# Kernel optimization log

Measured on AMD Instinct MI355X. Metric: run time of the kernel, lower is better.

Reference implementation:

```python
import jax, jax.numpy as jnp
import numpy as np

EPS = 1e-8

def unit_projection(x):
    # project each embedding vector so its Fourier coefficients have unit magnitude
    f = jnp.fft.fft(x, axis=-1)
    f = f / jnp.maximum(jnp.abs(f), EPS)
    return jnp.real(jnp.fft.ifft(f, axis=-1))

def bind(a, b):
    return jnp.fft.irfft(jnp.fft.rfft(a, axis=-1) * jnp.fft.rfft(b, axis=-1), n=a.shape[-1], axis=-1)

def unbind(s, k):
    # k is unit-magnitude in Fourier domain, so its inverse is its conjugate
    return jnp.fft.irfft(jnp.fft.rfft(s, axis=-1) * jnp.conj(jnp.fft.rfft(k, axis=-1)), n=s.shape[-1], axis=-1)

def layer_norm(x, g, b):
    mu = jnp.mean(x, axis=-1, keepdims=True)
    var = jnp.var(x, axis=-1, keepdims=True)
    return (x - mu) * jax.lax.rsqrt(var + 1e-5) * g + b

def setup_inputs():
    key = jax.random.key(0)
    ks = jax.random.split(key, 12)
    B, S, D = 4, 2048, 1024
    sc = 1.0 / np.sqrt(D)
    inp = {
        'x': jax.random.normal(ks[0], (B, S, D), jnp.float32),
        'Wq': jax.random.normal(ks[1], (D, D), jnp.float32) * sc,
        'bq': jnp.zeros((D,), jnp.float32),
        'Wk': jax.random.normal(ks[2], (D, D), jnp.float32) * sc,
        'bk': jnp.zeros((D,), jnp.float32),
        'Wv': jax.random.normal(ks[3], (D, D), jnp.float32) * sc,
        'bv': jnp.zeros((D,), jnp.float32),
        'ln1_g': jnp.ones((D,), jnp.float32), 'ln1_b': jnp.zeros((D,), jnp.float32),
        'ln2_g': jnp.ones((D,), jnp.float32), 'ln2_b': jnp.zeros((D,), jnp.float32),
        'W1': jax.random.normal(ks[4], (D, 4 * D), jnp.float32) * sc,
        'b1': jnp.zeros((4 * D,), jnp.float32),
        'W2': jax.random.normal(ks[5], (4 * D, D), jnp.float32) * (1.0 / np.sqrt(4 * D)),
        'b2': jnp.zeros((D,), jnp.float32),
    }
    return inp

def reference(x, Wq, bq, Wk, bk, Wv, bv, ln1_g, ln1_b, ln2_g, ln2_b, W1, b1, W2, b2):
    h = layer_norm(x, ln1_g, ln1_b)
    q = unit_projection(h @ Wq + bq)
    k = unit_projection(h @ Wk + bk)
    v = unit_projection(h @ Wv + bv)
    s = jnp.cumsum(bind(k, v), axis=1)  # causal prefix-sum over sequence
    mixed = unbind(s, q)
    x = x + mixed  # dropout=0.0
    h2 = layer_norm(x, ln2_g, ln2_b)
    mlp = jax.nn.gelu(h2 @ W1 + b1, approximate=False) @ W2 + b2
    return x + mlp
```

## Files before the change

kernel.cpp:

```cpp
#include <hip/hip_runtime.h>
#include <cstdint>
#include <cstddef>

#define DD 1024
#define SSEQ 2048
#define NB 4
#define MROWS 8192
#define FBINS 513
#define FPAD 520
#define WFP 1152
#define NQKV 3456
#define NHID 4096
#define NCHUNK 128
#define SCHUNK 16

typedef _Float16 f16_t;
typedef _Float16 f16x8 __attribute__((ext_vector_type(8)));
typedef _Float16 f16x2 __attribute__((ext_vector_type(2)));
typedef float f32x4 __attribute__((ext_vector_type(4)));

__device__ __forceinline__ float2 cmul(float2 a, float2 b) {
  return make_float2(a.x * b.x - a.y * b.y, a.x * b.y + a.y * b.x);
}

__device__ __forceinline__ void async_cp16(const void* g, void* l) {
  __builtin_amdgcn_global_load_lds(
      (const __attribute__((address_space(1))) void*)g,
      (__attribute__((address_space(3))) void*)l, 16, 0, 0);
}

template <int N> __device__ __forceinline__ void vwait();
template <> __device__ __forceinline__ void vwait<0>() { asm volatile("s_waitcnt vmcnt(0)" ::: "memory"); }
template <> __device__ __forceinline__ void vwait<1>() { asm volatile("s_waitcnt vmcnt(1)" ::: "memory"); }
template <> __device__ __forceinline__ void vwait<2>() { asm volatile("s_waitcnt vmcnt(2)" ::: "memory"); }
template <> __device__ __forceinline__ void vwait<3>() { asm volatile("s_waitcnt vmcnt(3)" ::: "memory"); }
template <> __device__ __forceinline__ void vwait<4>() { asm volatile("s_waitcnt vmcnt(4)" ::: "memory"); }
template <> __device__ __forceinline__ void vwait<5>() { asm volatile("s_waitcnt vmcnt(5)" ::: "memory"); }
template <> __device__ __forceinline__ void vwait<6>() { asm volatile("s_waitcnt vmcnt(6)" ::: "memory"); }

__device__ __forceinline__ float fast_gelu(float val) {
  float av = __builtin_fabsf(val);
  float z = av * 0.70710678118654752f;
  float t = __builtin_amdgcn_rcpf(__builtin_fmaf(0.3275911f, z, 1.0f));
  float poly = t * __builtin_fmaf(t,
      __builtin_fmaf(t, __builtin_fmaf(t,
          __builtin_fmaf(t, 1.061405429f, -1.453152027f),
          1.421413741f), -0.284496736f), 0.254829592f);
  float e = __builtin_amdgcn_exp2f(z * z * -1.4426950408889634f);
  float w = poly * e;
  float r = fmaxf(val, 0.0f);
  return __builtin_fmaf(-0.5f * av, w, r);
}

__device__ __forceinline__ void fft1024(float2* bufA, float2* bufB,
                                        const float2* tw, int lt) {
  float2* s = bufA;
  float2* d = bufB;
  for (int m = 1; m < 1024; m <<= 1) {
#pragma unroll
    for (int r2 = 0; r2 < 2; ++r2) {
      int u = lt + r2 * 256;
      int k = u & (m - 1);
      int jm = u - k;
      float2 c0 = s[u];
      float2 c1 = s[u + 512];
      float2 wt = tw[jm];
      float2 su = make_float2(c0.x + c1.x, c0.y + c1.y);
      float2 df = make_float2(c0.x - c1.x, c0.y - c1.y);
      float2 pr = cmul(wt, df);
      d[2 * jm + k] = su;
      d[2 * jm + k + m] = pr;
    }
    __syncthreads();
    float2* tmp = s; s = d; d = tmp;
  }
}

__device__ __forceinline__ float2* fft512(float2* bufA, float2* bufB,
                                          const float2* tw, int lt) {
  float2* s = bufA;
  float2* d = bufB;
  for (int m = 1; m < 512; m <<= 1) {
    int u = lt;
    int k = u & (m - 1);
    int jm = u - k;
    float2 c0 = s[u];
    float2 c1 = s[u + 256];
    float2 wt = tw[jm];
    float2 su = make_float2(c0.x + c1.x, c0.y + c1.y);
    float2 df = make_float2(c0.x - c1.x, c0.y - c1.y);
    float2 pr = cmul(wt, df);
    d[2 * jm + k] = su;
    d[2 * jm + k + m] = pr;
    __syncthreads();
    float2* tmp = s; s = d; d = tmp;
  }
  return s;
}

__global__ __launch_bounds__(512) void wfft_k(
    const float* __restrict__ Wq, const float* __restrict__ Wk,
    const float* __restrict__ Wv, const float* __restrict__ bq,
    const float* __restrict__ bk, const float* __restrict__ bv,
    float* __restrict__ WfAll, float* __restrict__ biasC) {
  __shared__ float2 tw[512];
  __shared__ float2 bufA[2][1024];
  __shared__ float2 bufB[2][1024];
  const int tid = threadIdx.x;
  const int rh = tid >> 8;
  const int lt = tid & 255;
  const int slot = blockIdx.x * 2 + rh;
  const float *src0, *src1;
  float *dstA, *dstB = nullptr;
  bool storeB = true;
  if (slot < 1536) {
    const int p = slot >> 9;
    const int j = slot & 511;
    const float* W = (p == 0) ? Wq : ((p == 1) ? Wk : Wv);
    src0 = W + (size_t)(2 * j) * DD;
    src1 = W + (size_t)(2 * j + 1) * DD;
    dstA = WfAll + ((size_t)p * DD + 2 * j) * WFP;
    dstB = WfAll + ((size_t)p * DD + 2 * j + 1) * WFP;
  } else if (slot == 1536) {
    src0 = bq; src1 = bk;
    dstA = biasC;
    dstB = biasC + WFP;
  } else {
    src0 = bv; src1 = bv;
    dstA = biasC + 2 * (size_t)WFP;
    storeB = false;
  }
  if (rh == 0) {
    for (int t = lt; t < 512; t += 256) {
      float ang = -6.2831853071795864769f * (float)t * (1.0f / 1024.0f);
      tw[t] = make_float2(cosf(ang), sinf(ang));
    }
  }
  for (int t = lt; t < 1024; t += 256)
    bufA[rh][t] = make_float2(src0[t], src1[t]);
  __syncthreads();
  fft1024(bufA[rh], bufB[rh], tw, lt);
  for (int k = lt; k <= 512; k += 256) {
    const int nk = (1024 - k) & 1023;
    const float2 zk = bufA[rh][k];
    const float2 zn = bufA[rh][nk];
    dstA[2 * k]     = 0.5f * (zk.x + zn.x);
    dstA[2 * k + 1] = 0.5f * (zk.y - zn.y);
    if (storeB) {
      dstB[2 * k]     = 0.5f * (zk.y + zn.y);
      dstB[2 * k + 1] = 0.5f * (zn.x - zk.x);
    }
  }
  for (int j = 1026 + lt; j < WFP; j += 256) {
    dstA[j] = 0.f;
    if (storeB) dstB[j] = 0.f;
  }
}

__global__ __launch_bounds__(256) void transpose_cast_qkv_k(
    const float* __restrict__ WfAll, f16_t* __restrict__ BtH) {
  __shared__ float tile[32][33];
  const int tx = threadIdx.x & 31, ty = threadIdx.x >> 5;
  const int n0 = blockIdx.x * 32, k0 = blockIdx.y * 32;
  const int pp = blockIdx.z;
  const float* W = WfAll + (size_t)pp * DD * WFP;
  f16_t* Wt = BtH + (size_t)pp * WFP * DD;
#pragma unroll
  for (int i = 0; i < 32; i += 8)
    tile[ty + i][tx] = W[(size_t)(k0 + ty + i) * WFP + n0 + tx];
  __syncthreads();
#pragma unroll
  for (int i = 0; i < 32; i += 8)
    Wt[(size_t)(n0 + ty + i) * DD + k0 + tx] = (f16_t)tile[tx][ty + i];
}

__global__ __launch_bounds__(256) void transpose_mlp_k(
    const float* __restrict__ W1, f16_t* __restrict__ W1T,
    const float* __restrict__ W2, f16_t* __restrict__ W2T) {
  __shared__ float tile[32][33];
  const int tx = threadIdx.x & 31, ty = threadIdx.x >> 5;
  const float* W; f16_t* Wt; int K, N, n0, k0;
  if (blockIdx.z == 0) {
    W = W1; Wt = W1T; K = DD; N = NHID;
    n0 = blockIdx.x * 32; k0 = blockIdx.y * 32;
  } else {
    W = W2; Wt = W2T; K = NHID; N = DD;
    n0 = blockIdx.y * 32; k0 = blockIdx.x * 32;
  }
#pragma unroll
  for (int i = 0; i < 32; i += 8)
    tile[ty + i][tx] = W[(size_t)(k0 + ty + i) * N + n0 + tx];
  __syncthreads();
#pragma unroll
  for (int i = 0; i < 32; i += 8)
    Wt[(size_t)(n0 + ty + i) * K + k0 + tx] = (f16_t)tile[tx][ty + i];
}

__global__ __launch_bounds__(256) void ln_cast_k(
    const float* __restrict__ x, const float* __restrict__ g,
    const float* __restrict__ b, f16_t* __restrict__ hH) {
  const int row = blockIdx.x, tid = threadIdx.x;
  __shared__ float red[8];
  const float* xr = x + (size_t)row * DD;
  float v[4], ls = 0.f, lq = 0.f;
#pragma unroll
  for (int i = 0; i < 4; ++i) {
    v[i] = xr[i * 256 + tid];
    ls += v[i];
    lq += v[i] * v[i];
  }
#pragma unroll
  for (int o = 32; o > 0; o >>= 1) {
    ls += __shfl_down(ls, o);
    lq += __shfl_down(lq, o);
  }
  const int lane = tid & 63, w = tid >> 6;
  if (lane == 0) { red[w] = ls; red[w + 4] = lq; }
  __syncthreads();
  const float S = red[0] + red[1] + red[2] + red[3];
  const float Q = red[4] + red[5] + red[6] + red[7];
  const float mean = S * (1.f / 1024.f);
  const float var = Q * (1.f / 1024.f) - mean * mean;
  const float rs = rsqrtf(var + 1e-5f);
#pragma unroll
  for (int i = 0; i < 4; ++i) {
    int n = i * 256 + tid;
    float val = (v[i] - mean) * rs * g[n] + b[n];
    hH[(size_t)row * DD + n] = (f16_t)val;
  }
}

__global__ __launch_bounds__(256, 3) void gemm_qkv_k(
    const f16_t* __restrict__ A, const f16_t* __restrict__ Bt,
    const float* __restrict__ bias, float* __restrict__ outF) {
  __shared__ alignas(16) f16_t AsH[128 * 64];
  __shared__ alignas(16) f16_t BsH[128 * 64];
  const int tid = threadIdx.x;
  const int lane = tid & 63;
  const int w = tid >> 6;
  const int wm = w >> 1, wn = w & 1;

  const int lin = blockIdx.x;
  const int s = (lin & 7) * 216 + (lin >> 3);
  const int g = s / 108;
  const int r = s % 108;
  const int n = r >> 2;
  const int m0 = g * 4 + (r & 3);
  const int bn = n * 128;
  const int bm = m0 * 128;

  f32x4 acc[4][4];
#pragma unroll
  for (int i = 0; i < 4; ++i)
#pragma unroll
    for (int j = 0; j < 4; ++j) acc[i][j] = (f32x4){0.f, 0.f, 0.f, 0.f};

  const int srow = lane >> 3;
  const int slot = lane & 7;

  for (int kt = 0; kt < 1024; kt += 64) {
#pragma unroll
    for (int i = 0; i < 4; ++i) {
      const int rb = (i * 4 + w) * 8;
      const int row = rb + srow;
      const int gg = (slot - (row & 7)) & 7;
      size_t ga = (size_t)(bm + row) * 1024 + kt + gg * 8;
      size_t gb = (size_t)(bn + row) * 1024 + kt + gg * 8;
      async_cp16(A + ga, &AsH[rb * 64]);
      async_cp16(Bt + gb, &BsH[rb * 64]);
    }
    __syncthreads();
#pragma unroll
    for (int ks = 0; ks < 2; ++ks) {
      const int cgbase = ks * 4 + (lane >> 4);
      f16x8 ah[4], bh[4];
#pragma unroll
      for (int mt = 0; mt < 4; ++mt) {
        int m = wm * 64 + mt * 16 + (lane & 15);
        int sl = (cgbase + (m & 7)) & 7;
        ah[mt] = *(const f16x8*)(&AsH[m * 64 + sl * 8]);
      }
#pragma unroll
      for (int nt = 0; nt < 4; ++nt) {
        int nn = wn * 64 + nt * 16 + (lane & 15);
        int sl = (cgbase + (nn & 7)) & 7;
        bh[nt] = *(const f16x8*)(&BsH[nn * 64 + sl * 8]);
      }
#pragma unroll
      for (int mt = 0; mt < 4; ++mt)
#pragma unroll
        for (int nt = 0; nt < 4; ++nt)
          acc[mt][nt] = __builtin_amdgcn_mfma_f32_16x16x32_f16(
              ah[mt], bh[nt], acc[mt][nt], 0, 0, 0);
    }
    __syncthreads();
  }

  const int q = lane >> 4;
  const int cn = lane & 15;
#pragma unroll
  for (int mt = 0; mt < 4; ++mt) {
#pragma unroll
    for (int nt = 0; nt < 4; ++nt) {
      const int gcol = bn + wn * 64 + nt * 16 + cn;
      const float bv = bias[gcol];
      const int grow0 = bm + wm * 64 + mt * 16 + q * 4;
#pragma unroll
      for (int i = 0; i < 4; ++i) {
        size_t idx = (size_t)(grow0 + i) * NQKV + gcol;
        outF[idx] = acc[mt][nt][i] + bv;
      }
    }
  }
}

template <int RHALF>
__device__ __forceinline__ void stage_half(const f16_t* __restrict__ G,
                                           int grow0, int ldk, int kt,
                                           f16_t* ls, int w, int lane) {
  const int srow = lane >> 3;
  const int slot = lane & 7;
#pragma unroll
  for (int j = 0; j < RHALF / 64; ++j) {
    const int rb = (w + j * 8) * 8;
    const int row = rb + srow;
    const int gg = (slot - (row & 7)) & 7;
    async_cp16(G + (size_t)(grow0 + row) * ldk + kt + gg * 8, ls + rb * 64);
  }
}

template <int BM, int BN>
__device__ __forceinline__ void readA(const f16_t* As, int mq, int wm, int lane,
                                      f16x8 (&aR)[BM / 64][2]) {
#pragma unroll
  for (int mf = 0; mf < BM / 64; ++mf) {
    const int m = mq * (BM / 2) + wm * (BM / 4) + mf * 16 + (lane & 15);
#pragma unroll
    for (int ks = 0; ks < 2; ++ks) {
      const int cg = ks * 4 + (lane >> 4);
      const int sl = (cg + (m & 7)) & 7;
      aR[mf][ks] = *(const f16x8*)(As + m * 64 + sl * 8);
    }
  }
}

template <int BM, int BN>
__device__ __forceinline__ void readB(const f16_t* Bs, int nq, int wn, int lane,
                                      f16x8 (&bR)[BN / 128][2]) {
#pragma unroll
  for (int nf = 0; nf < BN / 128; ++nf) {
    const int n = nq * (BN / 2) + wn * (BN / 8) + nf * 16 + (lane & 15);
#pragma unroll
    for (int ks = 0; ks < 2; ++ks) {
      const int cg = ks * 4 + (lane >> 4);
      const int sl = (cg + (n & 7)) & 7;
      bR[nf][ks] = *(const f16x8*)(Bs + n * 64 + sl * 8);
    }
  }
}

template <int MF, int NF>
__device__ __forceinline__ void mfma_q(f32x4 (&acc)[MF][NF],
                                       const f16x8 (&aR)[MF][2],
                                       const f16x8 (&bR)[NF][2]) {
#pragma unroll
  for (int ks = 0; ks < 2; ++ks)
#pragma unroll
    for (int mf = 0; mf < MF; ++mf)
#pragma unroll
      for (int nf = 0; nf < NF; ++nf)
        acc[mf][nf] = __builtin_amdgcn_mfma_f32_16x16x32_f16(
            aR[mf][ks], bR[nf][ks], acc[mf][nf], 0, 0, 0);
}

template <int BM, int BN, int MM, int NN, int KK, int EPI>
__global__ __launch_bounds__(512, 2) void gemm8p_k(
    const f16_t* __restrict__ A, const f16_t* __restrict__ Bt,
    const float* __restrict__ bias, const float* __restrict__ resid,
    float* __restrict__ outF, f16_t* __restrict__ outH) {
  constexpr int MF = BM / 64;
  constexpr int NF = BN / 128;
  constexpr int LA = BM / 128;
  constexpr int LB = BN / 128;
  constexpr int NT = KK / 64;
  constexpr int NI = NT / 2;
  constexpr int WAITN = LA + 2 * LB;
  constexpr int HT = (BM + BN) * 64;
  __shared__ alignas(16) f16_t lds[2 * HT];

  const int tid = threadIdx.x;
  const int lane = tid & 63;
  const int w = tid >> 6;
  const int wm = w >> 2;
  const int wn = w & 3;

  constexpr int ntm = MM / BM, ntn = NN / BN;
  constexpr int per = (ntm * ntn) / 8;
  const int lin = (int)blockIdx.x;
  const int s = (lin & 7) * per + (lin >> 3);
  const int bn = (s % ntn) * BN;
  const int bm = (s / ntn) * BM;

  f16_t* EA = lds;              f16_t* EB = lds + BM * 64;
  f16_t* OA = lds + HT;         f16_t* OB = lds + HT + BM * 64;

  f32x4 acc[2][2][MF][NF];
#pragma unroll
  for (int a0 = 0; a0 < 2; ++a0)
#pragma unroll
    for (int a1 = 0; a1 < 2; ++a1)
#pragma unroll
      for (int mf = 0; mf < MF; ++mf)
#pragma unroll
        for (int nf = 0; nf < NF; ++nf)
          acc[a0][a1][mf][nf] = (f32x4){0.f, 0.f, 0.f, 0.f};

  stage_half<BM / 2>(A, bm, KK, 0, EA, w, lane);
  stage_half<BN / 2>(Bt, bn, KK, 0, EB, w, lane);
  stage_half<BN / 2>(Bt, bn + BN / 2, KK, 0, EB + (BN / 2) * 64, w, lane);
  stage_half<BM / 2>(A, bm + BM / 2, KK, 0, EA + (BM / 2) * 64, w, lane);
  stage_half<BM / 2>(A, bm, KK, 64, OA, w, lane);
  stage_half<BN / 2>(Bt, bn, KK, 64, OB, w, lane);
  stage_half<BN / 2>(Bt, bn + BN / 2, KK, 64, OB + (BN / 2) * 64, w, lane);
  vwait<WAITN>();
  __builtin_amdgcn_s_barrier();

  f16x8 aR[MF][2], bR0[NF][2], bR1[NF][2];

  for (int i = 0; i < NI; ++i) {
    const bool pre = (i + 1 < NI);
    const int k1 = (2 * i + 1) << 6;
    const int k2 = (2 * i + 2) << 6;
    const int k3 = (2 * i + 3) << 6;

    readA<BM, BN>(EA, 0, wm, lane, aR);
    readB<BM, BN>(EB, 0, wn, lane, bR0);
    stage_half<BM / 2>(A, bm + BM / 2, KK, k1, OA + (BM / 2) * 64, w, lane);
    __builtin_amdgcn_s_barrier();
    __builtin_amdgcn_s_setprio(1);
    mfma_q<MF, NF>(acc[0][0], aR, bR0);
    __builtin_amdgcn_s_setprio(0);
    __builtin_amdgcn_s_barrier();

    readB<BM, BN>(EB, 1, wn, lane, bR1);
    if (pre) stage_half<BM / 2>(A, bm, KK, k2, EA, w, lane);
    __builtin_amdgcn_s_barrier();
    __builtin_amdgcn_s_setprio(1);
    mfma_q<MF, NF>(acc[0][1], aR, bR1);
    __builtin_amdgcn_s_setprio(0);
    __builtin_amdgcn_s_barrier();

    readA<BM, BN>(EA, 1, wm, lane, aR);
    if (pre) stage_half<BN / 2>(Bt, bn, KK, k2, EB, w, lane);
    __builtin_amdgcn_s_barrier();
    __builtin_amdgcn_s_setprio(1);
    mfma_q<MF, NF>(acc[1][0], aR, bR0);
    __builtin_amdgcn_s_setprio(0);
    __builtin_amdgcn_s_barrier();

    if (pre) stage_half<BN / 2>(Bt, bn + BN / 2, KK, k2,
                                EB + (BN / 2) * 64, w, lane);
    __builtin_amdgcn_s_barrier();
    __builtin_amdgcn_s_setprio(1);
    mfma_q<MF, NF>(acc[1][1], aR, bR1);
    __builtin_amdgcn_s_setprio(0);
    if (pre) vwait<WAITN>(); else vwait<0>();
    __builtin_amdgcn_s_barrier();

    readA<BM, BN>(OA, 0, wm, lane, aR);
    readB<BM, BN>(OB, 0, wn, lane, bR0);
    if (pre) stage_half<BM / 2>(A, bm + BM / 2, KK, k2,
                                EA + (BM / 2) * 64, w, lane);
    __builtin_amdgcn_s_barrier();
    __builtin_amdgcn_s_setprio(1);
    mfma_q<MF, NF>(acc[0][0], aR, bR0);
    __builtin_amdgcn_s_setprio(0);
    __builtin_amdgcn_s_barrier();

    readB<BM, BN>(OB, 1, wn, lane, bR1);
    if (pre) stage_half<BM / 2>(A, bm, KK, k3, OA, w, lane);
    __builtin_amdgcn_s_barrier();
    __builtin_amdgcn_s_setprio(1);
    mfma_q<MF, NF>(acc[0][1], aR, bR1);
    __builtin_amdgcn_s_setprio(0);
    __builtin_amdgcn_s_barrier();

    readA<BM, BN>(OA, 1, wm, lane, aR);
    if (pre) stage_half<BN / 2>(Bt, bn, KK, k3, OB, w, lane);
    __builtin_amdgcn_s_barrier();
    __builtin_amdgcn_s_setprio(1);
    mfma_q<MF, NF>(acc[1][0], aR, bR0);
    __builtin_amdgcn_s_setprio(0);
    __builtin_amdgcn_s_barrier();

    if (pre) stage_half<BN / 2>(Bt, bn + BN / 2, KK, k3,
                                OB + (BN / 2) * 64, w, lane);
    __builtin_amdgcn_s_barrier();
    __builtin_amdgcn_s_setprio(1);
    mfma_q<MF, NF>(acc[1][1], aR, bR1);
    __builtin_amdgcn_s_setprio(0);
    if (pre) vwait<WAITN>();
    __builtin_amdgcn_s_barrier();
  }

  const int q4 = lane >> 4;
  const int cn = lane & 15;
#pragma unroll
  for (int mq = 0; mq < 2; ++mq)
#pragma unroll
    for (int nq = 0; nq < 2; ++nq)
#pragma unroll
      for (int mf = 0; mf < MF; ++mf)
#pragma unroll
        for (int nf = 0; nf < NF; ++nf) {
          const int gcol = bn + nq * (BN / 2) + wn * (BN / 8) + nf * 16 + cn;
          const float bv = bias[gcol];
          const int grow0 = bm + mq * (BM / 2) + wm * (BM / 4) + mf * 16 + q4 * 4;
#pragma unroll
          for (int i = 0; i < 4; ++i) {
            const float val = acc[mq][nq][mf][nf][i] + bv;
            const size_t idx = (size_t)(grow0 + i) * NN + gcol;
            if (EPI == 1) {
              outH[idx] = (f16_t)fast_gelu(val);
            } else {
              outF[idx] = val + resid[idx];
            }
          }
        }
}

__device__ __forceinline__ float2 unitc(float2 a) {
  float inv = 1.0f / fmaxf(sqrtf(a.x * a.x + a.y * a.y), 1e-8f);
  return make_float2(a.x * inv, a.y * inv);
}
__device__ __forceinline__ float2 bind_bin(const float2* r, int f) {
  float2 kn = unitc(r[576 + f]);
  float2 vn = unitc(r[1152 + f]);
  return cmul(kn, vn);
}

__global__ __launch_bounds__(256) void scan_pass1_k(
    const float* __restrict__ qkvF, float2* __restrict__ T) {
  const int bid = blockIdx.x;
  const int sc = bid & (NCHUNK - 1);
  const int fh = (bid >> 7) & 1;
  const int b = bid >> 8;
  const int s0 = sc * SCHUNK;
  const float2* base = (const float2*)(qkvF + ((size_t)(b * SSEQ + s0)) * NQKV);
  for (int f = fh * 256 + threadIdx.x; f < FBINS; f += 512) {
    float2 acc = make_float2(0.f, 0.f);
    const float2* r = base;
    for (int i = 0; i < SCHUNK; ++i) {
      float2 pv = bind_bin(r, f);
      acc.x += pv.x; acc.y += pv.y;
      r += NQKV / 2;
    }
    T[((size_t)b * NCHUNK + sc) * FBINS + f] = acc;
  }
}

__global__ __launch_bounds__(256) void scan_pass2_k(float2* __restrict__ T) {
  const int wv = threadIdx.x >> 6, lane = threadIdx.x & 63;
  const int bin = blockIdx.x * 4 + wv;
  const int b = bin / FBINS, f = bin % FBINS;
  const size_t a0 = ((size_t)b * NCHUNK + 2 * lane) * FBINS + f;
  const size_t a1 = ((size_t)b * NCHUNK + 2 * lane + 1) * FBINS + f;
  float2 c0 = T[a0];
  float2 c1 = T[a1];
  float2 v = make_float2(c0.x + c1.x, c0.y + c1.y);
#pragma unroll
  for (int o = 1; o < 64; o <<= 1) {
    float vx = __shfl_up(v.x, o);
    float vy = __shfl_up(v.y, o);
    if (lane >= o) { v.x += vx; v.y += vy; }
  }
  float ex = __shfl_up(v.x, 1);
  float ey = __shfl_up(v.y, 1);
  if (lane == 0) { ex = 0.f; ey = 0.f; }
  T[a0] = make_float2(ex, ey);
  T[a1] = make_float2(ex + c0.x, ey + c0.y);
}

__global__ __launch_bounds__(256) void scan_pass3_k(
    const float* __restrict__ qkvF, const float2* __restrict__ T,
    float2* __restrict__ Scum) {
  const int bid = blockIdx.x;
  const int sc = bid & (NCHUNK - 1);
  const int fh = (bid >> 7) & 1;
  const int b = bid >> 8;
  const int s0 = sc * SCHUNK;
  const float2* base = (const float2*)(qkvF + ((size_t)(b * SSEQ + s0)) * NQKV);
  for (int f = fh * 256 + threadIdx.x; f < FBINS; f += 512) {
    float2 acc = T[((size_t)b * NCHUNK + sc) * FBINS + f];
    const float2* r = base;
    size_t orow = ((size_t)(b * SSEQ + s0)) * FPAD + f;
    for (int i = 0; i < SCHUNK; ++i) {
      float2 pv = bind_bin(r, f);
      acc.x += pv.x; acc.y += pv.y;
      Scum[orow] = acc;
      r += NQKV / 2;
      orow += FPAD;
    }
  }
}

__global__ __launch_bounds__(512) void unbind_ln2_k(
    const float2* __restrict__ Scum, const float* __restrict__ qkvF,
    const float* __restrict__ x, float* __restrict__ x2out,
    f16_t* __restrict__ h2, const float* __restrict__ g2,
    const float* __restrict__ b2) {
  __shared__ float2 tw[256];
  __shared__ float2 Marr[2][513];
  __shared__ float2 bufA[2][512];
  __shared__ float2 bufB[2][512];
  __shared__ float red[2][8];
  const int tid = threadIdx.x;
  const int rh = tid >> 8;
  const int lt = tid & 255;
  const int row = blockIdx.x * 2 + rh;

  if (rh == 0) {
    float ang = 6.2831853071795864769f * (float)lt * (1.0f / 512.0f);
    tw[lt] = make_float2(cosf(ang), sinf(ang));
  }
  const float2* qrow = (const float2*)(qkvF + (size_t)row * NQKV);
  for (int t = lt; t <= 512; t += 256) {
    float2 sc = Scum[(size_t)row * FPAD + t];
    float2 fq = unitc(qrow[t]);
    Marr[rh][t] = make_float2(sc.x * fq.x + sc.y * fq.y,
                              sc.y * fq.x - sc.x * fq.y);
  }
  __syncthreads();
#pragma unroll
  for (int rr = 0; rr < 2; ++rr) {
    int t = lt + rr * 256;
    float2 a = Marr[rh][t];
    float2 b = Marr[rh][512 - t];
    float2 E = make_float2(0.5f * (a.x + b.x), 0.5f * (a.y - b.y));
    float2 Dd = make_float2(0.5f * (a.x - b.x), 0.5f * (a.y + b.y));
    float ang = 6.2831853071795864769f * (float)t * (1.0f / 1024.0f);
    float cw = cosf(ang), sw = sinf(ang);
    float2 O = make_float2(cw * Dd.x - sw * Dd.y, cw * Dd.y + sw * Dd.x);
    bufA[rh][t] = make_float2(E.x - O.y, E.y + O.x);
  }
  __syncthreads();
  float2* res = fft512(bufA[rh], bufB[rh], tw, lt);

  const float* xr = x + (size_t)row * DD;
  float v[2][2];
  float ls = 0.f, lq = 0.f;
#pragma unroll
  for (int rr = 0; rr < 2; ++rr) {
    int n = lt + rr * 256;
    float2 z = res[n];
    float2 xv = *(const float2*)(xr + 2 * n);
    float v0 = xv.x + z.x * (1.0f / 512.0f);
    float v1 = xv.y + z.y * (1.0f / 512.0f);
    *(float2*)(x2out + (size_t)row * DD + 2 * n) = make_float2(v0, v1);
    v[rr][0] = v0; v[rr][1] = v1;
    ls += v0 + v1;
    lq += v0 * v0 + v1 * v1;
  }
#pragma unroll
  for (int o = 32; o > 0; o >>= 1) {
    ls += __shfl_down(ls, o);
    lq += __shfl_down(lq, o);
  }
  const int lane = tid & 63, w4 = (tid >> 6) & 3;
  if (lane == 0) { red[rh][w4] = ls; red[rh][w4 + 4] = lq; }
  __syncthreads();
  const float S = red[rh][0] + red[rh][1] + red[rh][2] + red[rh][3];
  const float Q = red[rh][4] + red[rh][5] + red[rh][6] + red[rh][7];
  const float mean = S * (1.f / 1024.f);
  const float var = Q * (1.f / 1024.f) - mean * mean;
  const float rs = rsqrtf(var + 1e-5f);
  f16_t* hr = h2 + (size_t)row * DD;
#pragma unroll
  for (int rr = 0; rr < 2; ++rr) {
    int n = lt + rr * 256;
    float2 gv = *(const float2*)(g2 + 2 * n);
    float2 bv = *(const float2*)(b2 + 2 * n);
    f16x2 hp;
    hp[0] = (f16_t)((v[rr][0] - mean) * rs * gv.x + bv.x);
    hp[1] = (f16_t)((v[rr][1] - mean) * rs * gv.y + bv.y);
    *(f16x2*)(hr + 2 * n) = hp;
  }
}

extern "C" void kernel_launch(void* const* d_in, const int* in_sizes, int n_in,
                              void* d_out, int out_size, void* d_ws,
                              size_t ws_size, hipStream_t stream) {
  const float* x     = (const float*)d_in[0];
  const float* Wq    = (const float*)d_in[1];
  const float* bq    = (const float*)d_in[2];
  const float* Wk    = (const float*)d_in[3];
  const float* bk    = (const float*)d_in[4];
  const float* Wv    = (const float*)d_in[5];
  const float* bv    = (const float*)d_in[6];
  const float* ln1_g = (const float*)d_in[7];
  const float* ln1_b = (const float*)d_in[8];
  const float* ln2_g = (const float*)d_in[9];
  const float* ln2_b = (const float*)d_in[10];
  const float* W1    = (const float*)d_in[11];
  const float* b1    = (const float*)d_in[12];
  const float* W2    = (const float*)d_in[13];
  const float* b2    = (const float*)d_in[14];
  float* out = (float*)d_out;

  char* p = (char*)d_ws;
  auto take = [&](size_t bytes) {
    char* r = p;
    p += (bytes + 255) & ~(size_t)255;
    return r;
  };
  f16_t* BtH   = (f16_t*)take((size_t)NQKV * DD * sizeof(f16_t));
  f16_t* W1T   = (f16_t*)take((size_t)NHID * DD * sizeof(f16_t));
  f16_t* W2T   = (f16_t*)take((size_t)DD * NHID * sizeof(f16_t));
  float* biasC = (float*)take((size_t)NQKV * sizeof(float));
  f16_t* hbuf  = (f16_t*)take((size_t)MROWS * DD * sizeof(f16_t));
  char*  big   = take((size_t)MROWS * NQKV * sizeof(float));
  float2* Scum = (float2*)take((size_t)MROWS * FPAD * sizeof(float2));
  float* x2    = (float*)take((size_t)MROWS * DD * sizeof(float));
  float2* Tch  = (float2*)take((size_t)NB * NCHUNK * FBINS * sizeof(float2));
  float* WfAll   = (float*)big;
  float* qkv_f   = (float*)big;
  f16_t* mlp1    = (f16_t*)big;

  wfft_k<<<769, 512, 0, stream>>>(Wq, Wk, Wv, bq, bk, bv, WfAll, biasC);
  transpose_cast_qkv_k<<<dim3(WFP / 32, DD / 32, 3), 256, 0, stream>>>(
      WfAll, BtH);
  transpose_mlp_k<<<dim3(128, 32, 2), 256, 0, stream>>>(W1, W1T, W2, W2T);

  ln_cast_k<<<MROWS, 256, 0, stream>>>(x, ln1_g, ln1_b, hbuf);

  gemm_qkv_k<<<(NQKV / 128) * (MROWS / 128), 256, 0, stream>>>(
      hbuf, BtH, biasC, qkv_f);

  scan_pass1_k<<<NB * NCHUNK * 2, 256, 0, stream>>>(qkv_f, Tch);
  scan_pass2_k<<<(NB * FBINS) / 4, 256, 0, stream>>>(Tch);
  scan_pass3_k<<<NB * NCHUNK * 2, 256, 0, stream>>>(qkv_f, Tch, Scum);

  unbind_ln2_k<<<MROWS / 2, 512, 0, stream>>>(Scum, qkv_f, x, x2, hbuf,
                                              ln2_g, ln2_b);

  gemm8p_k<256, 256, MROWS, NHID, DD, 1><<<512, 512, 0, stream>>>(
      hbuf, W1T, b1, nullptr, nullptr, mlp1);

  gemm8p_k<128, 256, MROWS, DD, NHID, 2><<<256, 512, 0, stream>>>(
      mlp1, W2T, b2, x2, out, nullptr);
}
```

Before: 472.6 us.

## Replace QKV GEMM and down-proj with double-buffered prefetch-two GEMM kernel

Adds a new templated GEMM kernel that uses two LDS buffers and stages tiles two K-steps ahead, with partial vmcnt waits and raised wave priority around the MFMA blocks. The QKV projection moves from a simple single-buffered 128x128 kernel with full barriers to this kernel using 256x128 tiles and 512 threads. The MLP down-projection also switches to it. The goal is to overlap global loads with matrix math and cut barrier stalls, in exchange for a more intricate wait-count schedule and a different tile shape for QKV.

New measurement: 496.3 us. +5.0%, slower.

```diff
diff --git a/kernel.cpp b/kernel.cpp
--- a/kernel.cpp
+++ b/kernel.cpp
@@ -230,90 +230,6 @@
   }
 }
 
-__global__ __launch_bounds__(256, 3) void gemm_qkv_k(
-    const f16_t* __restrict__ A, const f16_t* __restrict__ Bt,
-    const float* __restrict__ bias, float* __restrict__ outF) {
-  __shared__ alignas(16) f16_t AsH[128 * 64];
-  __shared__ alignas(16) f16_t BsH[128 * 64];
-  const int tid = threadIdx.x;
-  const int lane = tid & 63;
-  const int w = tid >> 6;
-  const int wm = w >> 1, wn = w & 1;
-
-  const int lin = blockIdx.x;
-  const int s = (lin & 7) * 216 + (lin >> 3);
-  const int g = s / 108;
-  const int r = s % 108;
-  const int n = r >> 2;
-  const int m0 = g * 4 + (r & 3);
-  const int bn = n * 128;
-  const int bm = m0 * 128;
-
-  f32x4 acc[4][4];
-#pragma unroll
-  for (int i = 0; i < 4; ++i)
-#pragma unroll
-    for (int j = 0; j < 4; ++j) acc[i][j] = (f32x4){0.f, 0.f, 0.f, 0.f};
-
-  const int srow = lane >> 3;
-  const int slot = lane & 7;
-
-  for (int kt = 0; kt < 1024; kt += 64) {
-#pragma unroll
-    for (int i = 0; i < 4; ++i) {
-      const int rb = (i * 4 + w) * 8;
-      const int row = rb + srow;
-      const int gg = (slot - (row & 7)) & 7;
-      size_t ga = (size_t)(bm + row) * 1024 + kt + gg * 8;
-      size_t gb = (size_t)(bn + row) * 1024 + kt + gg * 8;
-      async_cp16(A + ga, &AsH[rb * 64]);
-      async_cp16(Bt + gb, &BsH[rb * 64]);
-    }
-    __syncthreads();
-#pragma unroll
-    for (int ks = 0; ks < 2; ++ks) {
-      const int cgbase = ks * 4 + (lane >> 4);
-      f16x8 ah[4], bh[4];
-#pragma unroll
-      for (int mt = 0; mt < 4; ++mt) {
-        int m = wm * 64 + mt * 16 + (lane & 15);
-        int sl = (cgbase + (m & 7)) & 7;
-        ah[mt] = *(const f16x8*)(&AsH[m * 64 + sl * 8]);
-      }
-#pragma unroll
-      for (int nt = 0; nt < 4; ++nt) {
-        int nn = wn * 64 + nt * 16 + (lane & 15);
-        int sl = (cgbase + (nn & 7)) & 7;
-        bh[nt] = *(const f16x8*)(&BsH[nn * 64 + sl * 8]);
-      }
-#pragma unroll
-      for (int mt = 0; mt < 4; ++mt)
-#pragma unroll
-        for (int nt = 0; nt < 4; ++nt)
-          acc[mt][nt] = __builtin_amdgcn_mfma_f32_16x16x32_f16(
-              ah[mt], bh[nt], acc[mt][nt], 0, 0, 0);
-    }
-    __syncthreads();
-  }
-
-  const int q = lane >> 4;
-  const int cn = lane & 15;
-#pragma unroll
-  for (int mt = 0; mt < 4; ++mt) {
-#pragma unroll
-    for (int nt = 0; nt < 4; ++nt) {
-      const int gcol = bn + wn * 64 + nt * 16 + cn;
-      const float bv = bias[gcol];
-      const int grow0 = bm + wm * 64 + mt * 16 + q * 4;
-#pragma unroll
-      for (int i = 0; i < 4; ++i) {
-        size_t idx = (size_t)(grow0 + i) * NQKV + gcol;
-        outF[idx] = acc[mt][nt][i] + bv;
-      }
-    }
-  }
-}
-
 template <int RHALF>
 __device__ __forceinline__ void stage_half(const f16_t* __restrict__ G,
                                            int grow0, int ldk, int kt,
@@ -371,6 +287,35 @@
       for (int nf = 0; nf < NF; ++nf)
         acc[mf][nf] = __builtin_amdgcn_mfma_f32_16x16x32_f16(
             aR[mf][ks], bR[nf][ks], acc[mf][nf], 0, 0, 0);
+}
+
+template <int BM, int BN, int NN, int EPI, int MF, int NF>
+__device__ __forceinline__ void gemm_epilogue(
+    f32x4 (&acc)[2][2][MF][NF], int bm, int bn, int wm, int wn, int lane,
+    const float* __restrict__ bias, const float* __restrict__ resid,
+    float* __restrict__ outF, f16_t* __restrict__ outH) {
+  const int q4 = lane >> 4;
+  const int cn = lane & 15;
+#pragma unroll
+  for (int mq = 0; mq < 2; ++mq)
+#pragma unroll
+    for (int nq = 0; nq < 2; ++nq)
+#pragma unroll
+      for (int mf = 0; mf < MF; ++mf)
+#pragma unroll
+        for (int nf = 0; nf < NF; ++nf) {
+          const int gcol = bn + nq * (BN / 2) + wn * (BN / 8) + nf * 16 + cn;
+          const float bv = bias[gcol];
+          const int grow0 = bm + mq * (BM / 2) + wm * (BM / 4) + mf * 16 + q4 * 4;
+#pragma unroll
+          for (int i = 0; i < 4; ++i) {
+            const float val = acc[mq][nq][mf][nf][i] + bv;
+            const size_t idx = (size_t)(grow0 + i) * NN + gcol;
+            if (EPI == 1)      outH[idx] = (f16_t)fast_gelu(val);
+            else if (EPI == 2) outF[idx] = val + resid[idx];
+            else               outF[idx] = val;
+          }
+        }
 }
 
 template <int BM, int BN, int MM, int NN, int KK, int EPI>
@@ -503,30 +448,96 @@
     __builtin_amdgcn_s_barrier();
   }
 
-  const int q4 = lane >> 4;
-  const int cn = lane & 15;
-#pragma unroll
-  for (int mq = 0; mq < 2; ++mq)
-#pragma unroll
-    for (int nq = 0; nq < 2; ++nq)
+  gemm_epilogue<BM, BN, NN, EPI, MF, NF>(acc, bm, bn, wm, wn, lane,
+                                         bias, resid, outF, outH);
+}
+
+template <int BM, int BN, int MM, int NN, int KK, int EPI>
+__global__ __launch_bounds__(512, 2) void gemmft_k(
+    const f16_t* __restrict__ A, const f16_t* __restrict__ Bt,
+    const float* __restrict__ bias, const float* __restrict__ resid,
+    float* __restrict__ outF, f16_t* __restrict__ outH) {
+  constexpr int MF = BM / 64;
+  constexpr int NF = BN / 128;
+  constexpr int LA = BM / 128;
+  constexpr int LB = BN / 128;
+  constexpr int NT = KK / 64;
+  constexpr int PW = LA + 2 * LB;
+  constexpr int WN = 2 * LA + 2 * LB;
+  static_assert(WN == 6, "wait depth mismatch");
+  constexpr int HT = (BM + BN) * 64;
+  __shared__ alignas(16) f16_t lds[2 * HT];
+
+  const int tid = threadIdx.x;
+  const int lane = tid & 63;
+  const int w = tid >> 6;
+  const int wm = w >> 2;
+  const int wn = w & 3;
+
+  constexpr int ntm = MM / BM, ntn = NN / BN;
+  constexpr int per = (ntm * ntn) / 8;
+  const int lin = (int)blockIdx.x;
+  const int s = (lin & 7) * per + (lin >> 3);
+  const int bn = (s % ntn) * BN;
+  const int bm = (s / ntn) * BM;
+
+  f32x4 acc[2][2][MF][NF];
+#pragma unroll
+  for (int a0 = 0; a0 < 2; ++a0)
+#pragma unroll
+    for (int a1 = 0; a1 < 2; ++a1)
 #pragma unroll
       for (int mf = 0; mf < MF; ++mf)
 #pragma unroll
-        for (int nf = 0; nf < NF; ++nf) {
-          const int gcol = bn + nq * (BN / 2) + wn * (BN / 8) + nf * 16 + cn;
-          const float bv = bias[gcol];
-          const int grow0 = bm + mq * (BM / 2) + wm * (BM / 4) + mf * 16 + q4 * 4;
-#pragma unroll
-          for (int i = 0; i < 4; ++i) {
-            const float val = acc[mq][nq][mf][nf][i] + bv;
-            const size_t idx = (size_t)(grow0 + i) * NN + gcol;
-            if (EPI == 1) {
-              outH[idx] = (f16_t)fast_gelu(val);
-            } else {
-              outF[idx] = val + resid[idx];
-            }
-          }
-        }
+        for (int nf = 0; nf < NF; ++nf)
+          acc[a0][a1][mf][nf] = (f32x4){0.f, 0.f, 0.f, 0.f};
+
+  stage_half<BM / 2>(A, bm, KK, 0, lds, w, lane);
+  stage_half<BN>(Bt, bn, KK, 0, lds + BM * 64, w, lane);
+  stage_half<BM / 2>(A, bm + BM / 2, KK, 0, lds + (BM / 2) * 64, w, lane);
+  stage_half<BM / 2>(A, bm, KK, 64, lds + HT, w, lane);
+  stage_half<BN>(Bt, bn, KK, 64, lds + HT + BM * 64, w, lane);
+  vwait<PW>();
+  __builtin_amdgcn_s_barrier();
+
+  f16x8 aR[MF][2], bR0[NF][2], bR1[NF][2];
+
+  for (int t = 0; t < NT; ++t) {
+    f16_t* cur = lds + (t & 1) * HT;
+    f16_t* curB = cur + BM * 64;
+    f16_t* oth = lds + ((t + 1) & 1) * HT;
+    const bool p1 = (t + 1 < NT);
+    const bool p2 = (t + 2 < NT);
+
+    readA<BM, BN>(cur, 0, wm, lane, aR);
+    readB<BM, BN>(curB, 0, wn, lane, bR0);
+    readB<BM, BN>(curB, 1, wn, lane, bR1);
+    if (p1) stage_half<BM / 2>(A, bm + BM / 2, KK, (t + 1) << 6,
+                               oth + (BM / 2) * 64, w, lane);
+    __builtin_amdgcn_s_barrier();
+    __builtin_amdgcn_s_setprio(1);
+    mfma_q<MF, NF>(acc[0][0], aR, bR0);
+    mfma_q<MF, NF>(acc[0][1], aR, bR1);
+    __builtin_amdgcn_s_setprio(0);
+    if (p2) vwait<WN>(); else vwait<0>();
+    __builtin_amdgcn_s_barrier();
+
+    readA<BM, BN>(cur, 1, wm, lane, aR);
+    if (p2) {
+      stage_half<BM / 2>(A, bm, KK, (t + 2) << 6, cur, w, lane);
+      stage_half<BN>(Bt, bn, KK, (t + 2) << 6, curB, w, lane);
+    }
+    __builtin_amdgcn_s_barrier();
+    __builtin_amdgcn_s_setprio(1);
+    mfma_q<MF, NF>(acc[1][0], aR, bR0);
+    mfma_q<MF, NF>(acc[1][1], aR, bR1);
+    __builtin_amdgcn_s_setprio(0);
+    if (p2) vwait<WN>(); else vwait<0>();
+    __builtin_amdgcn_s_barrier();
+  }
+
+  gemm_epilogue<BM, BN, NN, EPI, MF, NF>(acc, bm, bn, wm, wn, lane,
+                                         bias, resid, outF, outH);
 }
 
 __device__ __forceinline__ float2 unitc(float2 a) {
@@ -733,8 +744,8 @@
 
   ln_cast_k<<<MROWS, 256, 0, stream>>>(x, ln1_g, ln1_b, hbuf);
 
-  gemm_qkv_k<<<(NQKV / 128) * (MROWS / 128), 256, 0, stream>>>(
-      hbuf, BtH, biasC, qkv_f);
+  gemmft_k<256, 128, MROWS, NQKV, DD, 3><<<864, 512, 0, stream>>>(
+      hbuf, BtH, biasC, nullptr, qkv_f, nullptr);
 
   scan_pass1_k<<<NB * NCHUNK * 2, 256, 0, stream>>>(qkv_f, Tch);
   scan_pass2_k<<<(NB * FBINS) / 4, 256, 0, stream>>>(Tch);
@@ -746,6 +757,6 @@
   gemm8p_k<256, 256, MROWS, NHID, DD, 1><<<512, 512, 0, stream>>>(
       hbuf, W1T, b1, nullptr, nullptr, mlp1);
 
-  gemm8p_k<128, 256, MROWS, DD, NHID, 2><<<256, 512, 0, stream>>>(
+  gemmft_k<128, 256, MROWS, DD, NHID, 2><<<256, 512, 0, stream>>>(
       mlp1, W2T, b2, x2, out, nullptr);
 }
```
